# Kernel optimization log

Hardware: AMD Instinct MI355X
Metric: run time of the kernel (lower is better)

Reference implementation:

```python
import jax, jax.numpy as jnp
import numpy as np

B, T, C = 2, 2048, 1024
H, D = 16, 64
EPS = 1e-6


def _layernorm(x, gamma, beta):
    # Faithful to the torch module: uses unbiased std (Bessel) and divides by (std + eps).
    mean = x.mean(-1, keepdims=True)
    std = jnp.sqrt(jnp.sum((x - mean) ** 2, axis=-1, keepdims=True) / (x.shape[-1] - 1))
    return gamma * (x - mean) / (std + EPS) + beta


def setup_inputs() -> dict:
    key = jax.random.key(0)
    ks = jax.random.split(key, 9)
    s = lambda fan_in: 1.0 / np.sqrt(fan_in)
    return {
        "x": jax.random.normal(ks[0], (B, T, C), dtype=jnp.float32),
        "qkv_w": jax.random.uniform(ks[1], (3 * C, C), jnp.float32, -s(C), s(C)),
        "proj_w": jax.random.uniform(ks[2], (C, C), jnp.float32, -s(C), s(C)),
        "proj_b": jax.random.uniform(ks[3], (C,), jnp.float32, -s(C), s(C)),
        "l1_w": jax.random.uniform(ks[4], (4 * C, C), jnp.float32, -s(C), s(C)),
        "l1_b": jax.random.uniform(ks[5], (4 * C,), jnp.float32, -s(C), s(C)),
        "l3_w": jax.random.uniform(ks[6], (C, 4 * C), jnp.float32, -s(4 * C), s(4 * C)),
        "l3_b": jax.random.uniform(ks[7], (C,), jnp.float32, -s(4 * C), s(4 * C)),
        "ln1_g": jnp.ones((C,), jnp.float32),
        "ln1_b": jnp.zeros((C,), jnp.float32),
        "ln2_g": jnp.ones((C,), jnp.float32),
        "ln2_b": jnp.zeros((C,), jnp.float32),
    }


def _attention(x, qkv_w, proj_w, proj_b):
    Bx, Tx, Cx = x.shape
    qkv = x @ qkv_w.T                      # [B,T,3C]
    q, k, v = jnp.split(qkv, 3, axis=-1)
    q = q.reshape(Bx, Tx, H, D)
    k = k.reshape(Bx, Tx, H, D)
    v = v.reshape(Bx, Tx, H, D)
    scores = jnp.einsum("bthd,bshd->bhts", q, k) * (D ** -0.5)  # [B,H,T,T]
    causal = jnp.tril(jnp.ones((Tx, Tx), dtype=bool))
    scores = jnp.where(causal, scores, -jnp.inf)
    attn = jax.nn.softmax(scores, axis=-1)
    out = jnp.einsum("bhts,bshd->bthd", attn, v).reshape(Bx, Tx, Cx)
    return out @ proj_w.T + proj_b


def _mlp(x, l1_w, l1_b, l3_w, l3_b):
    h = jax.nn.relu(x @ l1_w.T + l1_b)     # [B,T,4C]
    return h @ l3_w.T + l3_b


def reference(x, qkv_w, proj_w, proj_b, l1_w, l1_b, l3_w, l3_b, ln1_g, ln1_b, ln2_g, ln2_b):
    # Dropout is identity in eval mode.
    x1 = x + _attention(_layernorm(x, ln1_g, ln1_b), qkv_w, proj_w, proj_b)
    x2 = x1 + _mlp(_layernorm(x1, ln2_g, ln2_b), l1_w, l1_b, l3_w, l3_b)
    return x2
```

## Files before the change

### kernel.cpp

```cpp
#include <hip/hip_runtime.h>

typedef unsigned short u16;
typedef short short8 __attribute__((ext_vector_type(8)));
typedef float floatx4 __attribute__((ext_vector_type(4)));

#define TT 2048
#define CC 1024
#define QSCALE 0.1803368801111244f
#define MFIX 32.0f

__device__ __forceinline__ u16 f2bf(float f) {
  return (u16)((__float_as_uint(f) + 0x8000u) >> 16);
}

__device__ __forceinline__ unsigned int pk2bf(float a, float b) {
  unsigned int ua = __float_as_uint(a) + 0x8000u;
  unsigned int ub = __float_as_uint(b) + 0x8000u;
  return __builtin_amdgcn_perm(ub, ua, 0x07060302u);
}

__device__ __forceinline__ void glds16(const u16* g, u16* l) {
  __builtin_amdgcn_global_load_lds((const __attribute__((address_space(1))) void*)g,
                                   (__attribute__((address_space(3))) void*)l, 16, 0, 0);
}

__device__ __forceinline__ void ln_body(const float* __restrict__ x,
                                        const float* __restrict__ g,
                                        const float* __restrict__ b,
                                        u16* __restrict__ out, int row, int tid) {
  const float4* xr = (const float4*)(x + (size_t)row * CC);
  float4 v = xr[tid];
  float s = v.x + v.y + v.z + v.w;
  float sq = v.x * v.x + v.y * v.y + v.z * v.z + v.w * v.w;
#pragma unroll
  for (int off = 1; off < 64; off <<= 1) {
    s += __shfl_xor(s, off);
    sq += __shfl_xor(sq, off);
  }
  __shared__ float ss[4], ssq[4];
  int wave = tid >> 6;
  if ((tid & 63) == 0) { ss[wave] = s; ssq[wave] = sq; }
  __syncthreads();
  s = ss[0] + ss[1] + ss[2] + ss[3];
  sq = ssq[0] + ssq[1] + ssq[2] + ssq[3];
  float mean = s * (1.0f / CC);
  float var = (sq - (float)CC * mean * mean) * (1.0f / (CC - 1));
  float inv = 1.0f / (sqrtf(fmaxf(var, 0.0f)) + 1e-6f);
  float4 gv = ((const float4*)g)[tid];
  float4 bv = ((const float4*)b)[tid];
  ushort4 o;
  o.x = f2bf(gv.x * (v.x - mean) * inv + bv.x);
  o.y = f2bf(gv.y * (v.y - mean) * inv + bv.y);
  o.z = f2bf(gv.z * (v.z - mean) * inv + bv.z);
  o.w = f2bf(gv.w * (v.w - mean) * inv + bv.w);
  ((ushort4*)(out + (size_t)row * CC))[tid] = o;
}

__global__ __launch_bounds__(256) void cvt_ln_kernel(const float* __restrict__ w0,
                                                     const float* __restrict__ w1,
                                                     const float* __restrict__ w2,
                                                     const float* __restrict__ w3,
                                                     const float* __restrict__ x,
                                                     const float* __restrict__ lg,
                                                     const float* __restrict__ lb,
                                                     u16* __restrict__ o0,
                                                     u16* __restrict__ o1,
                                                     u16* __restrict__ o2,
                                                     u16* __restrict__ o3,
                                                     u16* __restrict__ oln) {
  int blk = blockIdx.x;
  if (blk >= 12288) {
    ln_body(x, lg, lb, oln, blk - 12288, threadIdx.x);
    return;
  }
  const float* in;
  u16* out;
  int base;
  if (blk < 3072)      { in = w0; out = o0; base = 0; }
  else if (blk < 4096) { in = w1; out = o1; base = 3072; }
  else if (blk < 8192) { in = w2; out = o2; base = 4096; }
  else                 { in = w3; out = o3; base = 8192; }
  int i = (blk - base) * 256 + threadIdx.x;
  float4 v = ((const float4*)in)[i];
  ushort4 o;
  o.x = f2bf(v.x); o.y = f2bf(v.y); o.z = f2bf(v.z); o.w = f2bf(v.w);
  ((ushort4*)out)[i] = o;
}

__global__ __launch_bounds__(256) void ln_kernel(const float* __restrict__ x,
                                                 const float* __restrict__ g,
                                                 const float* __restrict__ b,
                                                 u16* __restrict__ out) {
  ln_body(x, g, b, out, blockIdx.x, threadIdx.x);
}


#define STAGE(tt)                                                         \
  {                                                                       \
    _Pragma("unroll") for (int g_ = 0; g_ < G; g_++)                      \
        glds16(gptr[g_] + (size_t)(tt) * 64, &lds[(tt) % RING][ldd[g_]]); \
  }

#define BODY(t, VM)                                                       \
  {                                                                       \
    asm volatile("s_waitcnt vmcnt(" #VM ")" ::: "memory");                \
    __builtin_amdgcn_s_barrier();                                         \
    asm volatile("" ::: "memory");                                        \
    if ((t) + DEPTH < nst) STAGE((t) + DEPTH);                            \
    const u16* Ls = &lds[(t) % RING][0];                                  \
    _Pragma("unroll") for (int s_ = 0; s_ < 2; s_++) {                    \
      short8 bf[NJ];                                                      \
      _Pragma("unroll") for (int j_ = 0; j_ < NJ; j_++)                   \
          bf[j_] = *(const short8*)(Ls + (bOff[j_] ^ (s_ << 5)));         \
      _Pragma("unroll") for (int h_ = 0; h_ < MH; h_++) {                 \
        short8 af[MC];                                                    \
        _Pragma("unroll") for (int m_ = 0; m_ < MC; m_++)                 \
            af[m_] = *(const short8*)(Ls + (aOff[h_ * MC + m_] ^ (s_ << 5))); \
        if (MIDB && (s_ + h_ > 0)) __builtin_amdgcn_s_barrier();          \
        __builtin_amdgcn_s_setprio(1);                                    \
        _Pragma("unroll") for (int m_ = 0; m_ < MC; m_++)                 \
            _Pragma("unroll") for (int j_ = 0; j_ < NJ; j_++)             \
                acc[h_ * MC + m_][j_] = __builtin_amdgcn_mfma_f32_16x16x32_bf16( \
                    af[m_], bf[j_], acc[h_ * MC + m_][j_], 0, 0, 0);      \
        __builtin_amdgcn_s_setprio(0);                                    \
      }                                                                   \
    }                                                                     \
  }

template <int BM, int BN, int NWM, int NWN, int MODE, int DEPTH>
__global__ __launch_bounds__(64 * NWM * NWN, 2) void gemmp(
    const u16* __restrict__ A, const u16* __restrict__ W,
    const float* __restrict__ bias, const float* __restrict__ resid,
    float* __restrict__ outf, u16* __restrict__ outb,
    int M, int N, int K) {
  constexpr int NW = NWM * NWN;
  constexpr int MI = BM / NWM / 16;
  constexpr int NJ = BN / NWN / 16;
  constexpr int ROWS = BM + BN;
  constexpr int G = ROWS / 8 / NW;
  constexpr int MH = (MI > 4) ? 2 : 1;
  constexpr int MC = MI / MH;
  constexpr int RING = DEPTH + 1;
  constexpr bool MIDB = (NW == 8);
  static_assert(ROWS % (8 * NW) == 0, "chunk assignment");
  static_assert(DEPTH == 1 || G == 8, "counted vmcnt literal assumes G==8");
  __shared__ u16 lds[RING][ROWS * 64];

  const int tid = threadIdx.x;
  const int w = tid >> 6, lane = tid & 63;
  const int l15 = lane & 15, quad = lane >> 4;
  const int wm = (w / NWN) * (MI * 16);
  const int wn = (w % NWN) * (NJ * 16);
  const int tm = blockIdx.x * BM, tn = blockIdx.y * BN;

  const int srow = lane >> 3;
  const int xk = (lane & 7) ^ srow;
  const u16* gptr[G];
  int ldd[G];
#pragma unroll
  for (int g = 0; g < G; g++) {
    int c8 = (g * NW + w) * 8;
    const u16* rb = (c8 < BM) ? (A + (size_t)(tm + c8) * K)
                              : (W + (size_t)(tn + c8 - BM) * K);
    gptr[g] = rb + (size_t)srow * K + xk * 8;
    ldd[g] = c8 * 64;
  }

  int aOff[MI], bOff[NJ];
#pragma unroll
  for (int m = 0; m < MI; m++)
    aOff[m] = (wm + m * 16 + l15) * 64 + ((quad ^ (l15 & 7)) * 8);
#pragma unroll
  for (int j = 0; j < NJ; j++)
    bOff[j] = (BM + wn + j * 16 + l15) * 64 + ((quad ^ (l15 & 7)) * 8);

  floatx4 acc[MI][NJ];
#pragma unroll
  for (int m = 0; m < MI; m++)
#pragma unroll
    for (int j = 0; j < NJ; j++) acc[m][j] = (floatx4){0.f, 0.f, 0.f, 0.f};

  const int nst = K >> 6;

  STAGE(0);
  if constexpr (DEPTH == 2) STAGE(1);

  if constexpr (DEPTH == 1) {
#pragma unroll 2
    for (int t = 0; t < nst; ++t) BODY(t, 0);
  } else {
#pragma unroll 3
    for (int t = 0; t < nst - 1; ++t) BODY(t, 8);
    BODY(nst - 1, 0);
  }

  float bb[NJ];
#pragma unroll
  for (int j = 0; j < NJ; j++)
    bb[j] = (MODE == 1 || MODE == 2) ? bias[tn + wn + j * 16 + l15] : 0.0f;
#pragma unroll
  for (int m = 0; m < MI; m++) {
    int row0 = tm + wm + m * 16 + quad * 4;
#pragma unroll
    for (int j = 0; j < NJ; j++) {
      int col = tn + wn + j * 16 + l15;
#pragma unroll
      for (int r = 0; r < 4; r++) {
        float v = acc[m][j][r];
        size_t idx = (size_t)(row0 + r) * N + col;
        if (MODE == 0) {
          if (col < 1024) v *= QSCALE;
          outb[idx] = f2bf(v);
        } else if (MODE == 1) {
          outf[idx] = v + bb[j] + resid[idx];
        } else {
          outb[idx] = f2bf(fmaxf(v + bb[j], 0.0f));
        }
      }
    }
  }
}

#undef STAGE
#undef BODY

__global__ __launch_bounds__(256) void flash_kernel(const u16* __restrict__ qkv,
                                                    u16* __restrict__ attn) {
  int bid = blockIdx.x;
  int qt = 31 - (bid >> 5);
  int bh = bid & 31;
  int b = bh >> 4, h = bh & 15;
  int tid = threadIdx.x, w = tid >> 6, lane = tid & 63;
  int l15 = lane & 15, quad = lane >> 4;

  __shared__ u16 k_lds[128 * 64];
  __shared__ u16 vt_lds[64 * 128];
  __shared__ u16 p_lds[4][16 * 128];

  int qbase = qt * 64 + w * 16;
  const u16* qp = qkv + (size_t)(b * TT + qbase + l15) * 3072 + h * 64;
  short8 qf0 = *(const short8*)(qp + quad * 8);
  short8 qf1 = *(const short8*)(qp + 32 + quad * 8);

  float l_i = 0.0f;
  floatx4 accO[4];
#pragma unroll
  for (int jf = 0; jf < 4; jf++) accO[jf] = (floatx4){0.f, 0.f, 0.f, 0.f};

  int rsub = lane >> 3;
  int cg = (lane & 7) ^ rsub;
  const u16* Kg = qkv + (size_t)(b * TT + w * 32 + rsub) * 3072 + 1024 + h * 64 + cg * 8;
  u16* kL = k_lds + w * 32 * 64;
  int s4 = (tid & 31) * 4;
  int dg = (tid >> 5) * 8;
  const u16* Vg = qkv + (size_t)(b * TT + s4) * 3072 + 2048 + h * 64 + dg;
  int sl = s4 >> 3, so = s4 & 7;

  int x = l15 & 7;
  int kOff[8];
#pragma unroll
  for (int i = 0; i < 8; i++) kOff[i] = (i * 16 + l15) * 64 + ((quad ^ x) * 8);

  int nt = (qt + 2) >> 1;
  for (int kt = 0; kt < nt; kt++) {
    int s0 = kt * 128;
    size_t soff = (size_t)s0 * 3072;
    uint4 R0 = *(const uint4*)(Vg + soff);
    uint4 R1 = *(const uint4*)(Vg + soff + 3072);
    uint4 R2 = *(const uint4*)(Vg + soff + 6144);
    uint4 R3 = *(const uint4*)(Vg + soff + 9216);
    __syncthreads();
#pragma unroll
    for (int is = 0; is < 4; is++) glds16(Kg + soff + (size_t)is * 8 * 3072, kL + is * 512);
    {
      unsigned int a0[4] = {R0.x, R0.y, R0.z, R0.w};
      unsigned int a1[4] = {R1.x, R1.y, R1.z, R1.w};
      unsigned int a2[4] = {R2.x, R2.y, R2.z, R2.w};
      unsigned int a3[4] = {R3.x, R3.y, R3.z, R3.w};
#pragma unroll
      for (int p = 0; p < 4; p++) {
        uint2 ev, od;
        ev.x = __builtin_amdgcn_perm(a1[p], a0[p], 0x05040100u);
        ev.y = __builtin_amdgcn_perm(a3[p], a2[p], 0x05040100u);
        od.x = __builtin_amdgcn_perm(a1[p], a0[p], 0x07060302u);
        od.y = __builtin_amdgcn_perm(a3[p], a2[p], 0x07060302u);
        int r0 = dg + 2 * p, r1 = r0 + 1;
        *(uint2*)(vt_lds + r0 * 128 + ((sl ^ (r0 & 15)) << 3) + so) = ev;
        *(uint2*)(vt_lds + r1 * 128 + ((sl ^ (r1 & 15)) << 3) + so) = od;
      }
    }
    __syncthreads();

    floatx4 st[8];
#pragma unroll
    for (int i = 0; i < 8; i++) st[i] = (floatx4){0.f, 0.f, 0.f, 0.f};
#pragma unroll
    for (int i = 0; i < 8; i++) {
      short8 kf0 = *(const short8*)(k_lds + kOff[i]);
      short8 kf1 = *(const short8*)(k_lds + (kOff[i] ^ 32));
      st[i] = __builtin_amdgcn_mfma_f32_16x16x32_bf16(kf0, qf0, st[i], 0, 0, 0);
      st[i] = __builtin_amdgcn_mfma_f32_16x16x32_bf16(kf1, qf1, st[i], 0, 0, 0);
    }

    if (s0 + 127 > qbase) {
      int mg = qbase + l15;
#pragma unroll
      for (int i = 0; i < 8; i++)
#pragma unroll
        for (int r = 0; r < 4; r++) {
          int s = s0 + i * 16 + quad * 4 + r;
          if (s > mg) st[i][r] = -3.0e38f;
        }
    }

    float ts = 0.0f;
#pragma unroll
    for (int i = 0; i < 8; i++)
#pragma unroll
      for (int r = 0; r < 4; r++) {
        float p = __builtin_amdgcn_exp2f(st[i][r] - MFIX);
        st[i][r] = p;
        ts += p;
      }
    ts += __shfl_xor(ts, 16);
    ts += __shfl_xor(ts, 32);
    l_i += ts;

#pragma unroll
    for (int i = 0; i < 8; i++) {
      uint2 pk;
      pk.x = pk2bf(st[i][0], st[i][1]);
      pk.y = pk2bf(st[i][2], st[i][3]);
      *(uint2*)(p_lds[w] + l15 * 128 + (((2 * i + (quad >> 1)) ^ l15) << 3) +
                ((quad & 1) << 2)) = pk;
    }

    short8 pf[4];
#pragma unroll
    for (int c = 0; c < 4; c++)
      pf[c] = *(const short8*)(p_lds[w] + l15 * 128 + (((quad + 4 * c) ^ l15) << 3));
#pragma unroll
    for (int jf = 0; jf < 4; jf++) {
      int vRow = (jf * 16 + l15) * 128;
#pragma unroll
      for (int c = 0; c < 4; c++) {
        short8 vf = *(const short8*)(vt_lds + vRow + (((quad + 4 * c) ^ l15) << 3));
        accO[jf] = __builtin_amdgcn_mfma_f32_16x16x32_bf16(pf[c], vf, accO[jf], 0, 0, 0);
      }
    }
  }

  float invl = 1.0f / l_i;
  float iR[4];
#pragma unroll
  for (int r = 0; r < 4; r++) iR[r] = __shfl(invl, quad * 4 + r);
  int orow = b * TT + qbase + quad * 4;
#pragma unroll
  for (int r = 0; r < 4; r++) {
    u16* op = attn + (size_t)(orow + r) * CC + h * 64 + l15;
#pragma unroll
    for (int jf = 0; jf < 4; jf++) op[jf * 16] = f2bf(accO[jf][r] * iR[r]);
  }
}

extern "C" void kernel_launch(void* const* d_in, const int* in_sizes, int n_in,
                              void* d_out, int out_size, void* d_ws, size_t ws_size,
                              hipStream_t stream) {
  const float* x      = (const float*)d_in[0];
  const float* qkv_w  = (const float*)d_in[1];
  const float* proj_w = (const float*)d_in[2];
  const float* proj_b = (const float*)d_in[3];
  const float* l1_w   = (const float*)d_in[4];
  const float* l1_b   = (const float*)d_in[5];
  const float* l3_w   = (const float*)d_in[6];
  const float* l3_b   = (const float*)d_in[7];
  const float* ln1_g  = (const float*)d_in[8];
  const float* ln1_b  = (const float*)d_in[9];
  const float* ln2_g  = (const float*)d_in[10];
  const float* ln2_b  = (const float*)d_in[11];
  float* out = (float*)d_out;
  char* ws = (char*)d_ws;

  u16* w_qkv  = (u16*)(ws + 0);
  u16* w_proj = (u16*)(ws + 6291456);
  u16* w_l1   = (u16*)(ws + 8388608);
  u16* w_l3   = (u16*)(ws + 16777216);
  u16* lnb    = (u16*)(ws + 25165824);
  u16* qkvb   = (u16*)(ws + 33554432);
  u16* attnb  = (u16*)(ws + 58720256);
  float* x1   = (float*)(ws + 67108864);
  u16* hb     = (u16*)(ws + 83886080);

  cvt_ln_kernel<<<16384, 256, 0, stream>>>(qkv_w, proj_w, l1_w, l3_w, x, ln1_g, ln1_b,
                                           w_qkv, w_proj, w_l1, w_l3, lnb);
  gemmp<256, 256, 2, 4, 0, 1><<<dim3(16, 12), 512, 0, stream>>>(
      lnb, w_qkv, nullptr, nullptr, nullptr, qkvb, 4096, 3072, 1024);
  flash_kernel<<<1024, 256, 0, stream>>>(qkvb, attnb);
  gemmp<128, 128, 2, 2, 1, 2><<<dim3(32, 8), 256, 0, stream>>>(
      attnb, w_proj, proj_b, x, x1, nullptr, 4096, 1024, 1024);
  ln_kernel<<<4096, 256, 0, stream>>>(x1, ln2_g, ln2_b, lnb);
  gemmp<256, 256, 2, 4, 2, 1><<<dim3(16, 16), 512, 0, stream>>>(
      lnb, w_l1, l1_b, nullptr, nullptr, hb, 4096, 4096, 1024);
  gemmp<128, 128, 2, 2, 1, 2><<<dim3(32, 8), 256, 0, stream>>>(
      hb, w_l3, l3_b, x1, out, nullptr, 4096, 1024, 4096);
}
```

Before: 292.3 us.

## Add K=32 four-stage pipelined GEMM for QKV/MLP1 and shrink output GEMM tiles

Introduces a new gemm32 kernel for the QKV and first MLP GEMMs. It stages K in 32-wide slices through a 4-slot LDS ring with three loads in flight, uses counted vmcnt waits, and interleaves barriers with MFMA priority hints. This is meant to hide global-load latency better than the previous single-depth 64-wide pipeline. The projection and final MLP GEMMs switch to 128x64 tiles with twice as many blocks to improve CU occupancy, and the vmcnt literal is adjusted to match the new per-thread load count. The cost is extra per-iteration barriers and more redundant A-tile traffic.

```diff
diff --git a/kernel.cpp b/kernel.cpp
--- a/kernel.cpp
+++ b/kernel.cpp
@@ -143,7 +143,7 @@
   constexpr int RING = DEPTH + 1;
   constexpr bool MIDB = (NW == 8);
   static_assert(ROWS % (8 * NW) == 0, "chunk assignment");
-  static_assert(DEPTH == 1 || G == 8, "counted vmcnt literal assumes G==8");
+  static_assert(DEPTH == 1 || G == 6, "counted vmcnt literal assumes G==6");
   __shared__ u16 lds[RING][ROWS * 64];
 
   const int tid = threadIdx.x;
@@ -190,7 +190,7 @@
     for (int t = 0; t < nst; ++t) BODY(t, 0);
   } else {
 #pragma unroll 3
-    for (int t = 0; t < nst - 1; ++t) BODY(t, 8);
+    for (int t = 0; t < nst - 1; ++t) BODY(t, 6);
     BODY(nst - 1, 0);
   }
 
@@ -223,6 +223,116 @@
 
 #undef STAGE
 #undef BODY
+
+
+#define STG32(tt)                                                         \
+  {                                                                       \
+    _Pragma("unroll") for (int g_ = 0; g_ < 4; g_++)                      \
+        glds16(gptr[g_] + (size_t)(tt) * 32, &lds[(tt) & 3][ldd[g_]]);    \
+  }
+
+#define BODY32(t, VM)                                                     \
+  {                                                                       \
+    asm volatile("s_waitcnt vmcnt(" #VM ")" ::: "memory");                \
+    __builtin_amdgcn_s_barrier();                                         \
+    asm volatile("" ::: "memory");                                        \
+    if ((t) + 3 < nst) STG32((t) + 3);                                    \
+    const u16* Ls = &lds[(t) & 3][0];                                     \
+    short8 bf[4];                                                         \
+    _Pragma("unroll") for (int j_ = 0; j_ < 4; j_++)                      \
+        bf[j_] = *(const short8*)(Ls + bOff[j_]);                         \
+    _Pragma("unroll") for (int h_ = 0; h_ < 4; h_++) {                    \
+      short8 a0_ = *(const short8*)(Ls + aOff[2 * h_]);                   \
+      short8 a1_ = *(const short8*)(Ls + aOff[2 * h_ + 1]);               \
+      if (h_ > 0) __builtin_amdgcn_s_barrier();                           \
+      __builtin_amdgcn_s_setprio(1);                                      \
+      _Pragma("unroll") for (int j_ = 0; j_ < 4; j_++)                    \
+          acc[2 * h_][j_] = __builtin_amdgcn_mfma_f32_16x16x32_bf16(      \
+              a0_, bf[j_], acc[2 * h_][j_], 0, 0, 0);                     \
+      _Pragma("unroll") for (int j_ = 0; j_ < 4; j_++)                    \
+          acc[2 * h_ + 1][j_] = __builtin_amdgcn_mfma_f32_16x16x32_bf16(  \
+              a1_, bf[j_], acc[2 * h_ + 1][j_], 0, 0, 0);                 \
+      __builtin_amdgcn_s_setprio(0);                                      \
+    }                                                                     \
+  }
+
+template <int MODE>
+__global__ __launch_bounds__(512, 2) void gemm32(const u16* __restrict__ A,
+                                                 const u16* __restrict__ W,
+                                                 const float* __restrict__ bias,
+                                                 u16* __restrict__ outb,
+                                                 int M, int N, int K) {
+  __shared__ u16 lds[4][512 * 32];
+  const int tid = threadIdx.x;
+  const int w = tid >> 6, lane = tid & 63;
+  const int l15 = lane & 15, quad = lane >> 4;
+  const int wm = (w >> 2) * 128, wn = (w & 3) * 64;
+  const int tm = blockIdx.x * 256, tn = blockIdx.y * 256;
+
+  const int srow = lane >> 2;
+  const int xk = (lane & 3) ^ ((lane >> 3) & 3);
+  const u16* gptr[4];
+  int ldd[4];
+#pragma unroll
+  for (int g = 0; g < 4; g++) {
+    int c16 = (g * 8 + w) * 16;
+    const u16* rb = (c16 < 256) ? (A + (size_t)(tm + c16) * K)
+                                : (W + (size_t)(tn + c16 - 256) * K);
+    gptr[g] = rb + (size_t)srow * K + xk * 8;
+    ldd[g] = c16 * 32;
+  }
+
+  const int rsw = (quad ^ ((l15 >> 1) & 3)) * 8;
+  int aOff[8], bOff[4];
+#pragma unroll
+  for (int m = 0; m < 8; m++) aOff[m] = (wm + m * 16 + l15) * 32 + rsw;
+#pragma unroll
+  for (int j = 0; j < 4; j++) bOff[j] = (256 + wn + j * 16 + l15) * 32 + rsw;
+
+  floatx4 acc[8][4];
+#pragma unroll
+  for (int m = 0; m < 8; m++)
+#pragma unroll
+    for (int j = 0; j < 4; j++) acc[m][j] = (floatx4){0.f, 0.f, 0.f, 0.f};
+
+  const int nst = K >> 5;
+
+  STG32(0);
+  STG32(1);
+  STG32(2);
+
+#pragma unroll 4
+  for (int t = 0; t < nst - 2; ++t) BODY32(t, 8);
+  BODY32(nst - 2, 4);
+  BODY32(nst - 1, 0);
+
+  float bb[4];
+#pragma unroll
+  for (int j = 0; j < 4; j++)
+    bb[j] = (MODE == 2) ? bias[tn + wn + j * 16 + l15] : 0.0f;
+#pragma unroll
+  for (int m = 0; m < 8; m++) {
+    int row0 = tm + wm + m * 16 + quad * 4;
+#pragma unroll
+    for (int j = 0; j < 4; j++) {
+      int col = tn + wn + j * 16 + l15;
+#pragma unroll
+      for (int r = 0; r < 4; r++) {
+        float v = acc[m][j][r];
+        size_t idx = (size_t)(row0 + r) * N + col;
+        if (MODE == 0) {
+          if (col < 1024) v *= QSCALE;
+          outb[idx] = f2bf(v);
+        } else {
+          outb[idx] = f2bf(fmaxf(v + bb[j], 0.0f));
+        }
+      }
+    }
+  }
+}
+
+#undef STG32
+#undef BODY32
 
 __global__ __launch_bounds__(256) void flash_kernel(const u16* __restrict__ qkv,
                                                     u16* __restrict__ attn) {
@@ -393,14 +503,12 @@
 
   cvt_ln_kernel<<<16384, 256, 0, stream>>>(qkv_w, proj_w, l1_w, l3_w, x, ln1_g, ln1_b,
                                            w_qkv, w_proj, w_l1, w_l3, lnb);
-  gemmp<256, 256, 2, 4, 0, 1><<<dim3(16, 12), 512, 0, stream>>>(
-      lnb, w_qkv, nullptr, nullptr, nullptr, qkvb, 4096, 3072, 1024);
+  gemm32<0><<<dim3(16, 12), 512, 0, stream>>>(lnb, w_qkv, nullptr, qkvb, 4096, 3072, 1024);
   flash_kernel<<<1024, 256, 0, stream>>>(qkvb, attnb);
-  gemmp<128, 128, 2, 2, 1, 2><<<dim3(32, 8), 256, 0, stream>>>(
+  gemmp<128, 64, 2, 2, 1, 2><<<dim3(32, 16), 256, 0, stream>>>(
       attnb, w_proj, proj_b, x, x1, nullptr, 4096, 1024, 1024);
   ln_kernel<<<4096, 256, 0, stream>>>(x1, ln2_g, ln2_b, lnb);
-  gemmp<256, 256, 2, 4, 2, 1><<<dim3(16, 16), 512, 0, stream>>>(
-      lnb, w_l1, l1_b, nullptr, nullptr, hb, 4096, 4096, 1024);
-  gemmp<128, 128, 2, 2, 1, 2><<<dim3(32, 8), 256, 0, stream>>>(
+  gemm32<2><<<dim3(16, 16), 512, 0, stream>>>(lnb, w_l1, l1_b, hb, 4096, 4096, 1024);
+  gemmp<128, 64, 2, 2, 1, 2><<<dim3(32, 16), 256, 0, stream>>>(
       hb, w_l3, l3_b, x1, out, nullptr, 4096, 1024, 4096);
 }
```

Result: faster. 286.2 us (-2.1%).
